# Optimization experiments

Hardware: AMD Instinct MI355X
Metric: run time of the kernel (lower is better)

The kernel has to match this reference:

```python
import jax, jax.numpy as jnp
import numpy as np

K = 2  # pooling_size == pooling_stride == 2, pad == 0


def _maxpool2d_with_flat_indices(mu):
    """Non-overlapping 2x2 max pool returning pooled values and flat H*W argmax indices,
    matching torch.nn.functional.max_pool2d(..., return_indices=True)."""
    B, C, H, W = mu.shape
    Ho, Wo = H // K, W // K
    # [B,C,Ho,Wo,K*K] window view
    patches = mu.reshape(B, C, Ho, K, Wo, K).transpose(0, 1, 2, 4, 3, 5).reshape(B, C, Ho, Wo, K * K)
    mu_out = jnp.max(patches, axis=-1)                      # [B,C,Ho,Wo]
    w = jnp.argmax(patches, axis=-1)                        # in-window index 0..K*K-1
    row = jnp.arange(Ho)[:, None] * K + w // K              # [B,C,Ho,Wo]
    col = jnp.arange(Wo)[None, :] * K + w % K               # [B,C,Ho,Wo]
    flat = (row * W + col).reshape(B, C, Ho * Wo)           # [B,C,N], N = Ho*Wo
    return mu_out, flat


def setup_inputs() -> dict:
    key = jax.random.key(0)
    k1, k2 = jax.random.split(key)
    mu_in = jax.random.normal(k1, (8, 32, 32, 32), dtype=jnp.float32)
    Sigma_in = jax.random.normal(k2, (8, 32, 1024, 1024), dtype=jnp.float32)
    return {"mu_in": mu_in, "Sigma_in": Sigma_in}


def reference(mu_in, Sigma_in):
    mu_out, idx = _maxpool2d_with_flat_indices(mu_in)       # idx: [B,C,N]
    # Double gather: Sigma_out[b,c,i,j] = Sigma_in[b,c, idx[b,c,i], idx[b,c,j]]
    g1 = jnp.take_along_axis(Sigma_in, idx[:, :, :, None], axis=2)   # [B,C,N,HW]
    Sigma_out = jnp.take_along_axis(g1, idx[:, :, None, :], axis=3)  # [B,C,N,N]
    return mu_out, Sigma_out
```

## Files before the change

### kernel.cpp

```cpp
#include <hip/hip_runtime.h>
#include <hip/hip_bf16.h>


#define BC    256
#define H     32
#define W     32
#define HO    16
#define WO    16
#define NPOOL 256
#define HW    1024

__global__ void pool_idx_kernel(const float* __restrict__ mu_in,
                                float* __restrict__ mu_out,
                                int* __restrict__ idx_ws) {
    const int bc = blockIdx.x;
    const int n  = threadIdx.x;
    const int i  = n >> 4;
    const int j  = n & 15;

    const float* img = mu_in + (size_t)bc * (H * W);
    const int r0 = 2 * i, c0 = 2 * j;

    float v0 = img[(r0    ) * W + c0    ];
    float v1 = img[(r0    ) * W + c0 + 1];
    float v2 = img[(r0 + 1) * W + c0    ];
    float v3 = img[(r0 + 1) * W + c0 + 1];

    float best = v0; int w = 0;
    if (v1 > best) { best = v1; w = 1; }
    if (v2 > best) { best = v2; w = 2; }
    if (v3 > best) { best = v3; w = 3; }

    const int row = r0 + (w >> 1);
    const int col = c0 + (w & 1);
    const int flat = row * W + col;

    mu_out[(size_t)bc * NPOOL + n] = best;
    idx_ws[bc * NPOOL + n] = flat;
}

__global__ void sigma_gather_kernel(const float* __restrict__ Sigma_in,
                                    const int* __restrict__ idx_ws,
                                    float* __restrict__ Sigma_out) {
    const int blk = blockIdx.x;
    const int bc  = blk >> 8;
    const int i   = blk & 255;
    const int j   = threadIdx.x;

    const int* idx = idx_ws + bc * NPOOL;
    const int r  = idx[i];
    const int cj = idx[j];

    const float* srow = Sigma_in + (size_t)bc * HW * HW + (size_t)r * HW;
    const float  v    = srow[cj];

    Sigma_out[(size_t)bc * (NPOOL * NPOOL) + (size_t)i * NPOOL + j] = v;
}

extern "C" void kernel_launch(void* const* d_in, const int* in_sizes, int n_in,
                              void* d_out, int out_size, void* d_ws, size_t ws_size,
                              hipStream_t stream) {
    const float* mu_in    = (const float*)d_in[0];
    const float* Sigma_in = (const float*)d_in[1];

    float* mu_out    = (float*)d_out;
    float* Sigma_out = (float*)d_out + BC * NPOOL;
    int*   idx_ws    = (int*)d_ws;

    pool_idx_kernel<<<BC, NPOOL, 0, stream>>>(mu_in, mu_out, idx_ws);
    sigma_gather_kernel<<<BC * NPOOL, NPOOL, 0, stream>>>(Sigma_in, idx_ws, Sigma_out);
}
```

Measured before the change: 1.190 ms.

## Stage gathered Sigma rows through LDS with coalesced float4 loads per wave

```diff
diff --git a/kernel.cpp b/kernel.cpp
--- a/kernel.cpp
+++ b/kernel.cpp
@@ -1,5 +1,4 @@
 #include <hip/hip_runtime.h>
-#include <hip/hip_bf16.h>
 
 
 #define BC    256
@@ -39,22 +38,64 @@
     idx_ws[bc * NPOOL + n] = flat;
 }
 
-__global__ void sigma_gather_kernel(const float* __restrict__ Sigma_in,
-                                    const int* __restrict__ idx_ws,
-                                    float* __restrict__ Sigma_out) {
-    const int blk = blockIdx.x;
-    const int bc  = blk >> 8;
-    const int i   = blk & 255;
-    const int j   = threadIdx.x;
+#define ROWS_PER_WAVE   8
+#define WAVES_PER_BLOCK 4
+#define ROWS_PER_BLOCK  (ROWS_PER_WAVE * WAVES_PER_BLOCK)
+#define BLOCKS_PER_BC   (NPOOL / ROWS_PER_BLOCK)
 
-    const int* idx = idx_ws + bc * NPOOL;
-    const int r  = idx[i];
-    const int cj = idx[j];
+__global__ __launch_bounds__(256, 8)
+void sigma_gather_kernel(const float* __restrict__ Sigma_in,
+                         const int* __restrict__ idx_ws,
+                         float* __restrict__ Sigma_out) {
+    __shared__ int   s_idx[NPOOL];
+    __shared__ float s_row[WAVES_PER_BLOCK][HW];
 
-    const float* srow = Sigma_in + (size_t)bc * HW * HW + (size_t)r * HW;
-    const float  v    = srow[cj];
+    const int blk   = blockIdx.x;
+    const int bc    = blk >> 3;
+    const int chunk = blk & 7;
+    const int tid   = threadIdx.x;
+    const int wave  = tid >> 6;
+    const int lane  = tid & 63;
 
-    Sigma_out[(size_t)bc * (NPOOL * NPOOL) + (size_t)i * NPOOL + j] = v;
+    s_idx[tid] = idx_ws[bc * NPOOL + tid];
+    __syncthreads();
+
+    const float* Sbase = Sigma_in  + (size_t)bc * (HW * HW);
+    float*       Obase = Sigma_out + (size_t)bc * (NPOOL * NPOOL);
+
+    const int j0 = 4 * lane;
+    const int c0 = s_idx[j0 + 0];
+    const int c1 = s_idx[j0 + 1];
+    const int c2 = s_idx[j0 + 2];
+    const int c3 = s_idx[j0 + 3];
+
+    const int ibase = chunk * ROWS_PER_BLOCK + wave * ROWS_PER_WAVE;
+    float* rowbuf = s_row[wave];
+
+    #pragma unroll 2
+    for (int t = 0; t < ROWS_PER_WAVE; ++t) {
+        const int i = ibase + t;
+        const int r = s_idx[i];
+
+        const float4* src4 = (const float4*)(Sbase + (size_t)r * HW);
+        float4 v0 = src4[lane      ];
+        float4 v1 = src4[lane +  64];
+        float4 v2 = src4[lane + 128];
+        float4 v3 = src4[lane + 192];
+
+        float4* rb4 = (float4*)rowbuf;
+        rb4[lane      ] = v0;
+        rb4[lane +  64] = v1;
+        rb4[lane + 128] = v2;
+        rb4[lane + 192] = v3;
+
+        float4 o;
+        o.x = rowbuf[c0];
+        o.y = rowbuf[c1];
+        o.z = rowbuf[c2];
+        o.w = rowbuf[c3];
+        ((float4*)(Obase + (size_t)i * NPOOL))[lane] = o;
+    }
 }
 
 extern "C" void kernel_launch(void* const* d_in, const int* in_sizes, int n_in,
@@ -68,5 +109,5 @@
     int*   idx_ws    = (int*)d_ws;
 
     pool_idx_kernel<<<BC, NPOOL, 0, stream>>>(mu_in, mu_out, idx_ws);
-    sigma_gather_kernel<<<BC * NPOOL, NPOOL, 0, stream>>>(Sigma_in, idx_ws, Sigma_out);
+    sigma_gather_kernel<<<BC * BLOCKS_PER_BC, 256, 0, stream>>>(Sigma_in, idx_ws, Sigma_out);
 }
```

After: 1.205 ms. No clear change (+1.2%).
